# Optimization experiments

Measured on AMD Instinct MI355X. Metric: run time of the kernel, lower is better.

## Reference

```python
import jax, jax.numpy as jnp
import numpy as np

B, QL, KL, D, H = 2, 512, 8192, 1024, 8
HD = D // H  # head dim = 128


def setup_inputs() -> dict:
    key = jax.random.key(0)
    ks = jax.random.split(key, 12)
    s = 0.02
    return {
        "inputs_q": jax.random.normal(ks[0], (B, QL, D), jnp.float32),
        "inputs_k": jax.random.normal(ks[1], (B, KL, D), jnp.float32),
        "inputs_v": jax.random.normal(ks[2], (B, KL, D), jnp.float32),
        "attention_mask": jax.random.randint(ks[3], (B, QL, KL), 0, 2).astype(bool),
        "Wq": jax.random.normal(ks[4], (D, D), jnp.float32) * s,
        "bq": jnp.zeros((D,), jnp.float32),
        "Wk": jax.random.normal(ks[5], (D, D), jnp.float32) * s,
        "bk": jnp.zeros((D,), jnp.float32),
        "Wv": jax.random.normal(ks[6], (D, D), jnp.float32) * s,
        "bv": jnp.zeros((D,), jnp.float32),
        "Wf": jax.random.normal(ks[7], (D, D), jnp.float32) * s,
        "bf": jnp.zeros((D,), jnp.float32),
    }


def reference(inputs_q, inputs_k, inputs_v, attention_mask, Wq, bq, Wk, bk, Wv, bv, Wf, bf):
    # Projections (torch Linear: x @ W.T + b)
    q = inputs_q @ Wq.T + bq  # [B, QL, D]
    k = inputs_k @ Wk.T + bk  # [B, KL, D]
    v = inputs_v @ Wv.T + bv  # [B, KL, D]

    q = q.reshape(B, QL, H, HD)
    k = k.reshape(B, KL, H, HD)
    v = v.reshape(B, KL, H, HD)

    # scores [B, H, QL, KL]
    scores = jnp.einsum("bqhd,bkhd->bhqk", q, k)
    scale = 1.0 / np.sqrt(HD).astype(np.float32)
    scores = scores * scale
    large_k = jnp.float32(1e30)
    scores = jnp.where(attention_mask[:, None, :, :], scores, -large_k)

    probs = jax.nn.softmax(scores, axis=-1)
    # note: original calls self.dropout(normalized) but discards the result -> no-op

    summed = jnp.einsum("bhqk,bkhd->bqhd", probs, v).reshape(B, QL, H * HD)

    # wipe rows whose mask is all zero
    wipe = jnp.all(~attention_mask, axis=2, keepdims=True)  # [B, QL, 1]
    summed = jnp.where(wipe, jnp.zeros_like(summed), summed)

    return summed @ Wf.T + bf
```

## Files before the change

kernel.cpp:

```cpp
#include <hip/hip_runtime.h>
#include <hip/hip_bf16.h>
#include <math.h>

typedef __attribute__((ext_vector_type(4))) float fx4;
typedef __attribute__((ext_vector_type(4))) short sx4;
typedef __attribute__((ext_vector_type(8))) short sx8;
typedef unsigned long long u64;

#define MFMA16(a, b, c) __builtin_amdgcn_mfma_f32_16x16x16bf16_1k(a, b, c, 0, 0, 0)
#define MFMA32(a, b, c) __builtin_amdgcn_mfma_f32_16x16x32_bf16(a, b, c, 0, 0, 0)

__device__ __forceinline__ unsigned short f2bf(float f) {
  unsigned int u = __float_as_uint(f);
  return (unsigned short)((u + 0x7fffu + ((u >> 16) & 1u)) >> 16);
}

typedef const __attribute__((address_space(1))) char* gc1p;
typedef __attribute__((address_space(3))) char* lc3p;
__device__ __forceinline__ void glds16(const void* g, const void* lds_uniform) {
  gc1p gp = (gc1p)(unsigned long long)(uintptr_t)g;
  lc3p lp = (lc3p)(unsigned)__builtin_amdgcn_readfirstlane((int)(unsigned)(uintptr_t)lds_uniform);
  __builtin_amdgcn_global_load_lds(gp, lp, 16, 0, 0);
}

__global__ __launch_bounds__(256) void k_conv(const float* __restrict__ s,
                                              short* __restrict__ d) {
  size_t i = ((size_t)blockIdx.x * 256 + threadIdx.x) * 8;
  const fx4 a = *(const fx4*)(s + i);
  const fx4 b = *(const fx4*)(s + i + 4);
  sx8 o;
  o[0] = (short)f2bf(a[0]); o[1] = (short)f2bf(a[1]);
  o[2] = (short)f2bf(a[2]); o[3] = (short)f2bf(a[3]);
  o[4] = (short)f2bf(b[0]); o[5] = (short)f2bf(b[1]);
  o[6] = (short)f2bf(b[2]); o[7] = (short)f2bf(b[3]);
  *(sx8*)(d + i) = o;
}

__global__ __launch_bounds__(256) void k_conv_a(const float* ink, const float* inq,
                                                const float* Wq, const float* Wk,
                                                const float* Wv, const float* Wf,
                                                short* ck, short* cq, short* cwq,
                                                short* cwk, short* cwv, short* cwf) {
  int bx = blockIdx.x;
  const float* s;
  short* d;
  size_t i;
  if (bx < 8192) {
    s = ink; d = ck; i = (size_t)bx * 2048;
  } else {
    const int r = bx - 8192;
    const int seg = r >> 9;
    s = seg == 0 ? inq : seg == 1 ? Wq : seg == 2 ? Wk : seg == 3 ? Wv : Wf;
    d = seg == 0 ? cq : seg == 1 ? cwq : seg == 2 ? cwk : seg == 3 ? cwv : cwf;
    i = (size_t)(r & 511) * 2048;
  }
  i += (size_t)threadIdx.x * 8;
  const fx4 a = *(const fx4*)(s + i);
  const fx4 b = *(const fx4*)(s + i + 4);
  sx8 o;
  o[0] = (short)f2bf(a[0]); o[1] = (short)f2bf(a[1]);
  o[2] = (short)f2bf(a[2]); o[3] = (short)f2bf(a[3]);
  o[4] = (short)f2bf(b[0]); o[5] = (short)f2bf(b[1]);
  o[6] = (short)f2bf(b[2]); o[7] = (short)f2bf(b[3]);
  *(sx8*)(d + i) = o;
}

__global__ __launch_bounds__(256) void k_pack_mask(const int* __restrict__ mask,
                                                   u64* __restrict__ mb) {
  int g = blockIdx.x * 256 + threadIdx.x;
  u64 bal = __ballot(mask[g] != 0);
  if ((threadIdx.x & 63) == 0) mb[g >> 6] = bal;
}

template <int MODE>
__global__ __launch_bounds__(256) void k_gemm(const short* __restrict__ A,
                                              const short* __restrict__ Bw,
                                              const float* __restrict__ bias,
                                              void* __restrict__ Cptr,
                                              int M, int N, int K, float alpha) {
  __shared__ __align__(16) short sA[8192];
  __shared__ __align__(16) short sB[8192];
  const int t = threadIdx.x;
  const int lane = t & 63;
  const int w = t >> 6;
  const int quad = lane >> 4;
  const int l16 = lane & 15;
  const int x7 = l16 & 7;
  const int ntile = N >> 7;
  const int n0 = (blockIdx.x % ntile) << 7;
  const int m0 = (blockIdx.x / ntile) << 7;
  const int wm = (w >> 1) << 6;
  const int wn = (w & 1) << 6;
  const fx4 fzero = {0.f, 0.f, 0.f, 0.f};
  fx4 acc[4][4];
#pragma unroll
  for (int i = 0; i < 4; i++)
#pragma unroll
    for (int j = 0; j < 4; j++) acc[i][j] = fzero;

  const int srow = (lane >> 3);
  const int scb = lane & 7;

  for (int k0 = 0; k0 < K; k0 += 64) {
    __syncthreads();
#pragma unroll
    for (int j = 0; j < 4; j++) {
      const int row = w * 32 + j * 8 + srow;
      const int cb = scb ^ (row & 7);
      glds16(A + (size_t)(m0 + row) * K + k0 + cb * 8, &sA[(w * 32 + j * 8) * 64]);
      glds16(Bw + (size_t)(n0 + row) * K + k0 + cb * 8, &sB[(w * 32 + j * 8) * 64]);
    }
    __syncthreads();
#pragma unroll
    for (int kc = 0; kc < 2; kc++) {
      const int cbp = ((kc * 4 + quad) ^ x7) * 8;
      sx8 fa[4], fb[4];
#pragma unroll
      for (int i = 0; i < 4; i++) {
        fa[i] = *(const sx8*)(&sA[(wm + i * 16 + l16) * 64 + cbp]);
        fb[i] = *(const sx8*)(&sB[(wn + i * 16 + l16) * 64 + cbp]);
      }
#pragma unroll
      for (int mi = 0; mi < 4; mi++)
#pragma unroll
        for (int ni = 0; ni < 4; ni++)
          acc[mi][ni] = MFMA32(fa[mi], fb[ni], acc[mi][ni]);
    }
  }
#pragma unroll
  for (int ni = 0; ni < 4; ni++) {
    const int col = n0 + wn + ni * 16 + l16;
    const float bval = bias[col];
    if (MODE == 2) {
#pragma unroll
      for (int mi = 0; mi < 4; mi++) {
        const int rowb = m0 + wm + mi * 16 + quad * 4;
        const int bb = rowb >> 13;
        const int kl = (rowb & 8191) ^ ((col & 8) ? 4 : 0);
        sx4 pkv;
#pragma unroll
        for (int r = 0; r < 4; r++) pkv[r] = (short)f2bf(acc[mi][ni][r] + bval);
        *(sx4*)((unsigned short*)Cptr + ((size_t)bb * 1024 + col) * 8192 + kl) = pkv;
      }
    } else {
#pragma unroll
      for (int mi = 0; mi < 4; mi++)
#pragma unroll
        for (int r = 0; r < 4; r++) {
          const int row = m0 + wm + mi * 16 + quad * 4 + r;
          const float v = (acc[mi][ni][r] + bval) * alpha;
          if (MODE == 1) ((float*)Cptr)[(size_t)row * N + col] = v;
          else ((unsigned short*)Cptr)[(size_t)row * N + col] = f2bf(v);
        }
    }
  }
}

__global__ __launch_bounds__(256, 4) void k_attn(const short* __restrict__ Qp,
                                                 const short* __restrict__ Kp,
                                                 const short* __restrict__ Vt,
                                                 const u64* __restrict__ mb,
                                                 float* __restrict__ ml,
                                                 float* __restrict__ Op) {
  __shared__ __align__(16) short sK[8192];
  __shared__ __align__(16) short sV[8192];
  const int x = blockIdx.x;
  const int s = x & 7;
  const int qt = (x >> 3) & 7;
  const int h = (x >> 6) & 7;
  const int b = x >> 9;
  const int t = threadIdx.x;
  const int lane = t & 63;
  const int w = t >> 6;
  const int quad = lane >> 4;
  const int l16 = lane & 15;
  const int x7 = l16 & 7;
  const int q0 = qt << 6;
  const fx4 fzero = {0.f, 0.f, 0.f, 0.f};

  const short* qbase = Qp + (size_t)(b * 512 + q0 + w * 16 + l16) * 1024 + h * 128;
  sx8 aq[4];
#pragma unroll
  for (int kc = 0; kc < 4; kc++) aq[kc] = *(const sx8*)(qbase + kc * 32 + quad * 8);

  fx4 Ot[8];
#pragma unroll
  for (int d = 0; d < 8; d++) Ot[d] = fzero;
  float lsum = 0.f;

  const short* kbase = Kp + (size_t)(b * 8192 + s * 1024) * 1024 + h * 128;
  const short* vbase = Vt + (size_t)(b * 1024 + h * 128) * 8192 + s * 1024;
  const u64* wdp = mb + (size_t)(b * 512 + q0 + w * 16 + l16) * 128 + s * 16;
  const int srow4 = lane >> 4, scb16 = lane & 15;
  const int srow8 = lane >> 3, scb8 = lane & 7;
  const int h4 = ((quad & 1) ^ ((l16 >> 3) & 1)) * 4;

  for (int kt = 0; kt < 16; kt++) {
    __syncthreads();
#pragma unroll
    for (int j = 0; j < 4; j++) {
      const int row = (w * 4 + j) * 4 + srow4;
      const int cb = scb16 ^ (row & 7);
      glds16(kbase + (size_t)(kt * 64 + row) * 1024 + cb * 8, &sK[(w * 4 + j) * 512]);
    }
#pragma unroll
    for (int j = 0; j < 4; j++) {
      const int row = (w * 4 + j) * 8 + srow8;
      const int cb = scb8 ^ (row & 7);
      glds16(vbase + (size_t)row * 8192 + kt * 64 + cb * 8, &sV[(w * 4 + j) * 512]);
    }
    const u64 wd = wdp[kt];
    __syncthreads();
    const unsigned lo = (unsigned)wd, hi = (unsigned)(wd >> 32);
    sx4 pk[4];
#pragma unroll
    for (int nt = 0; nt < 4; nt++) {
      fx4 a = fzero;
#pragma unroll
      for (int kc = 0; kc < 4; kc++) {
        const sx8 kf = *(const sx8*)(&sK[(nt * 16 + l16) * 128 + ((kc * 4 + quad) ^ x7) * 8]);
        a = MFMA32(kf, aq[kc], a);
      }
      const unsigned bits = (nt & 2) ? hi : lo;
      const int sh = (nt & 1) * 16 + quad * 4;
      float pv[4];
#pragma unroll
      for (int r = 0; r < 4; r++) {
        const float e = __builtin_amdgcn_exp2f(a[r]);
        pv[r] = ((bits >> (sh + r)) & 1u) ? e : 0.f;
        lsum += pv[r];
      }
      sx4 pko;
      ((unsigned*)&pko)[0] = __builtin_amdgcn_perm(
          __float_as_uint(pv[1]) + 0x8000u, __float_as_uint(pv[0]) + 0x8000u, 0x07060302u);
      ((unsigned*)&pko)[1] = __builtin_amdgcn_perm(
          __float_as_uint(pv[3]) + 0x8000u, __float_as_uint(pv[2]) + 0x8000u, 0x07060302u);
      pk[nt] = pko;
    }
#pragma unroll
    for (int dt = 0; dt < 8; dt++) {
      fx4 o = Ot[dt];
#pragma unroll
      for (int nt = 0; nt < 4; nt++) {
        const int cb = (2 * nt + (quad >> 1)) ^ x7;
        const sx4 vf = *(const sx4*)(&sV[(dt * 16 + l16) * 64 + cb * 8 + h4]);
        o = MFMA16(vf, pk[nt], o);
      }
      Ot[dt] = o;
    }
  }
  lsum += __shfl_xor(lsum, 16, 64);
  lsum += __shfl_xor(lsum, 32, 64);
  if (lane < 16) ml[(size_t)x * 64 + w * 16 + l16] = lsum;
  float* ob = Op + (size_t)x * 8192 + (w * 16 + l16) * 128 + quad * 4;
#pragma unroll
  for (int dt = 0; dt < 8; dt++) *(fx4*)(ob + dt * 16) = Ot[dt];
}

__global__ __launch_bounds__(256) void k_combine(const float* __restrict__ ml,
                                                 const float* __restrict__ Op,
                                                 short* __restrict__ summed) {
  const int xc = blockIdx.x;
  const int qt = xc & 7;
  const int h = (xc >> 3) & 7;
  const int b = xc >> 6;
  const int t = threadIdx.x;
  const int row = t >> 2;
  const int dg = (t & 3) * 32;
  float L = 0.f;
#pragma unroll
  for (int s = 0; s < 8; s++) L += ml[(size_t)(xc * 8 + s) * 64 + row];
  float o[32];
#pragma unroll
  for (int i = 0; i < 32; i++) o[i] = 0.f;
  if (L != 0.f) {
#pragma unroll
    for (int s = 0; s < 8; s++) {
      const float* src = Op + (size_t)(xc * 8 + s) * 8192 + row * 128 + dg;
#pragma unroll
      for (int i = 0; i < 8; i++) {
        const fx4 v = *(const fx4*)(src + i * 4);
        o[i * 4 + 0] += v[0]; o[i * 4 + 1] += v[1];
        o[i * 4 + 2] += v[2]; o[i * 4 + 3] += v[3];
      }
    }
    const float inv = 1.f / L;
#pragma unroll
    for (int i = 0; i < 32; i++) o[i] *= inv;
  }
  short* dst = summed + (size_t)(b * 512 + qt * 64 + row) * 1024 + h * 128 + dg;
#pragma unroll
  for (int i = 0; i < 4; i++) {
    sx8 pkv;
#pragma unroll
    for (int j = 0; j < 8; j++) pkv[j] = (short)f2bf(o[i * 8 + j]);
    *(sx8*)(dst + i * 8) = pkv;
  }
}

extern "C" void kernel_launch(void* const* d_in, const int* in_sizes, int n_in,
                              void* d_out, int out_size, void* d_ws, size_t ws_size,
                              hipStream_t stream) {
  (void)in_sizes; (void)n_in; (void)out_size; (void)ws_size;
  const float* inq = (const float*)d_in[0];
  const float* ink = (const float*)d_in[1];
  const float* inv = (const float*)d_in[2];
  const int* mask = (const int*)d_in[3];
  const float* Wq = (const float*)d_in[4];
  const float* bq = (const float*)d_in[5];
  const float* Wk = (const float*)d_in[6];
  const float* bk = (const float*)d_in[7];
  const float* Wv = (const float*)d_in[8];
  const float* bv = (const float*)d_in[9];
  const float* Wf = (const float*)d_in[10];
  const float* bf = (const float*)d_in[11];

  char* ws = (char*)d_ws;
  short* S1 = (short*)(ws + 0);
  short* S2 = (short*)(ws + 33554432);
  short* S3 = (short*)(ws + 67108864);
  short* cq = (short*)(ws + 100663296);
  short* cwq = (short*)(ws + 102760448);
  short* cwk = (short*)(ws + 104857600);
  short* cwv = (short*)(ws + 106954752);
  short* cwf = (short*)(ws + 109051904);
  short* Qp = (short*)(ws + 111149056);
  short* summed = (short*)(ws + 113246208);
  u64* mb = (u64*)(ws + 115343360);
  float* ml = (float*)(ws + 116391936);

  const float alpha_q = 0.12751757f;

  k_conv_a<<<10752, 256, 0, stream>>>(ink, inq, Wq, Wk, Wv, Wf, S1, cq, cwq, cwk, cwv, cwf);
  k_pack_mask<<<32768, 256, 0, stream>>>(mask, mb);
  k_gemm<0><<<1024, 256, 0, stream>>>(S1, cwk, bk, S2, 16384, 1024, 1024, 1.f);
  k_conv<<<8192, 256, 0, stream>>>(inv, S1);
  k_gemm<2><<<1024, 256, 0, stream>>>(S1, cwv, bv, S3, 16384, 1024, 1024, 1.f);
  k_gemm<0><<<64, 256, 0, stream>>>(cq, cwq, bq, Qp, 1024, 1024, 1024, alpha_q);
  k_attn<<<1024, 256, 0, stream>>>(Qp, S2, S3, mb, ml, (float*)S1);
  k_combine<<<128, 256, 0, stream>>>(ml, (const float*)S1, summed);
  k_gemm<1><<<64, 256, 0, stream>>>(summed, cwf, bf, (float*)d_out, 1024, 1024, 1024, 1.f);
}
```

Before: 428.1 us.

## Merge prep kernels, fuse V and Q projections, use smaller tiles and remap attention blocks

```diff
diff --git a/kernel.cpp b/kernel.cpp
--- a/kernel.cpp
+++ b/kernel.cpp
@@ -21,6 +21,54 @@
   gc1p gp = (gc1p)(unsigned long long)(uintptr_t)g;
   lc3p lp = (lc3p)(unsigned)__builtin_amdgcn_readfirstlane((int)(unsigned)(uintptr_t)lds_uniform);
   __builtin_amdgcn_global_load_lds(gp, lp, 16, 0, 0);
+}
+
+__global__ __launch_bounds__(256) void k_prep(
+    const float* __restrict__ ink, const float* __restrict__ inq,
+    const float* __restrict__ Wq, const float* __restrict__ Wk,
+    const float* __restrict__ Wv, const float* __restrict__ Wf,
+    const int* __restrict__ mask, short* ck, short* cq, short* cwq, short* cwk,
+    short* cwv, short* cwf, u64* __restrict__ mb) {
+  __shared__ unsigned char nib[256];
+  const int bx = blockIdx.x;
+  const int t = threadIdx.x;
+  if (bx >= 10752) {
+    const int mbx = bx - 10752;
+    const int4 m = *(const int4*)(mask + (size_t)mbx * 1024 + t * 4);
+    nib[t] = (unsigned char)((m.x != 0) | ((m.y != 0) << 1) | ((m.z != 0) << 2) |
+                             ((m.w != 0) << 3));
+    __syncthreads();
+    if (t < 16) {
+      u64 wv = 0;
+#pragma unroll
+      for (int i = 0; i < 16; i++) wv |= (u64)(nib[t * 16 + i] & 0xF) << (4 * i);
+      mb[(size_t)mbx * 16 + t] = wv;
+    }
+    return;
+  }
+  const float* s;
+  short* d;
+  size_t i;
+  if (bx < 8192) {
+    s = ink; d = ck; i = (size_t)bx * 2048;
+  } else if (bx < 8704) {
+    s = inq; d = cq; i = (size_t)(bx - 8192) * 2048;
+  } else {
+    const int r = bx - 8704;
+    const int seg = r >> 9;
+    s = seg == 0 ? Wq : seg == 1 ? Wk : seg == 2 ? Wv : Wf;
+    d = seg == 0 ? cwq : seg == 1 ? cwk : seg == 2 ? cwv : cwf;
+    i = (size_t)(r & 511) * 2048;
+  }
+  i += (size_t)t * 8;
+  const fx4 a = *(const fx4*)(s + i);
+  const fx4 b = *(const fx4*)(s + i + 4);
+  sx8 o;
+  o[0] = (short)f2bf(a[0]); o[1] = (short)f2bf(a[1]);
+  o[2] = (short)f2bf(a[2]); o[3] = (short)f2bf(a[3]);
+  o[4] = (short)f2bf(b[0]); o[5] = (short)f2bf(b[1]);
+  o[6] = (short)f2bf(b[2]); o[7] = (short)f2bf(b[3]);
+  *(sx8*)(d + i) = o;
 }
 
 __global__ __launch_bounds__(256) void k_conv(const float* __restrict__ s,
@@ -36,50 +84,13 @@
   *(sx8*)(d + i) = o;
 }
 
-__global__ __launch_bounds__(256) void k_conv_a(const float* ink, const float* inq,
-                                                const float* Wq, const float* Wk,
-                                                const float* Wv, const float* Wf,
-                                                short* ck, short* cq, short* cwq,
-                                                short* cwk, short* cwv, short* cwf) {
-  int bx = blockIdx.x;
-  const float* s;
-  short* d;
-  size_t i;
-  if (bx < 8192) {
-    s = ink; d = ck; i = (size_t)bx * 2048;
-  } else {
-    const int r = bx - 8192;
-    const int seg = r >> 9;
-    s = seg == 0 ? inq : seg == 1 ? Wq : seg == 2 ? Wk : seg == 3 ? Wv : Wf;
-    d = seg == 0 ? cq : seg == 1 ? cwq : seg == 2 ? cwk : seg == 3 ? cwv : cwf;
-    i = (size_t)(r & 511) * 2048;
-  }
-  i += (size_t)threadIdx.x * 8;
-  const fx4 a = *(const fx4*)(s + i);
-  const fx4 b = *(const fx4*)(s + i + 4);
-  sx8 o;
-  o[0] = (short)f2bf(a[0]); o[1] = (short)f2bf(a[1]);
-  o[2] = (short)f2bf(a[2]); o[3] = (short)f2bf(a[3]);
-  o[4] = (short)f2bf(b[0]); o[5] = (short)f2bf(b[1]);
-  o[6] = (short)f2bf(b[2]); o[7] = (short)f2bf(b[3]);
-  *(sx8*)(d + i) = o;
-}
-
-__global__ __launch_bounds__(256) void k_pack_mask(const int* __restrict__ mask,
-                                                   u64* __restrict__ mb) {
-  int g = blockIdx.x * 256 + threadIdx.x;
-  u64 bal = __ballot(mask[g] != 0);
-  if ((threadIdx.x & 63) == 0) mb[g >> 6] = bal;
-}
-
-template <int MODE>
-__global__ __launch_bounds__(256) void k_gemm(const short* __restrict__ A,
-                                              const short* __restrict__ Bw,
-                                              const float* __restrict__ bias,
-                                              void* __restrict__ Cptr,
-                                              int M, int N, int K, float alpha) {
-  __shared__ __align__(16) short sA[8192];
-  __shared__ __align__(16) short sB[8192];
+template <int MODE, int MT>
+__device__ __forceinline__ void gemm_body(short* sA, short* sB,
+                                          const short* __restrict__ A,
+                                          const short* __restrict__ Bw,
+                                          const float* __restrict__ bias,
+                                          void* __restrict__ Cptr, int M, int N,
+                                          int K, float alpha, int bx) {
   const int t = threadIdx.x;
   const int lane = t & 63;
   const int w = t >> 6;
@@ -87,48 +98,64 @@
   const int l16 = lane & 15;
   const int x7 = l16 & 7;
   const int ntile = N >> 7;
-  const int n0 = (blockIdx.x % ntile) << 7;
-  const int m0 = (blockIdx.x / ntile) << 7;
-  const int wm = (w >> 1) << 6;
-  const int wn = (w & 1) << 6;
+  const int n0 = (bx % ntile) << 7;
+  const int m0 = (bx / ntile) * MT;
+  constexpr int NI = (MT == 128) ? 4 : 2;
+  const int wm = (MT == 128) ? ((w >> 1) << 6) : 0;
+  const int wn = (MT == 128) ? ((w & 1) << 6) : (w << 5);
   const fx4 fzero = {0.f, 0.f, 0.f, 0.f};
-  fx4 acc[4][4];
+  fx4 acc[4][NI];
 #pragma unroll
   for (int i = 0; i < 4; i++)
 #pragma unroll
-    for (int j = 0; j < 4; j++) acc[i][j] = fzero;
-
-  const int srow = (lane >> 3);
+    for (int j = 0; j < NI; j++) acc[i][j] = fzero;
+
+  const int srow = lane >> 3;
   const int scb = lane & 7;
 
   for (int k0 = 0; k0 < K; k0 += 64) {
     __syncthreads();
+    if (MT == 128) {
+#pragma unroll
+      for (int j = 0; j < 4; j++) {
+        const int row = w * 32 + j * 8 + srow;
+        const int cb = scb ^ (row & 7);
+        glds16(A + (size_t)(m0 + row) * K + k0 + cb * 8, &sA[(w * 32 + j * 8) * 64]);
+      }
+    } else {
+#pragma unroll
+      for (int j = 0; j < 2; j++) {
+        const int row = j * 32 + w * 8 + srow;
+        const int cb = scb ^ (row & 7);
+        glds16(A + (size_t)(m0 + row) * K + k0 + cb * 8, &sA[(j * 32 + w * 8) * 64]);
+      }
+    }
 #pragma unroll
     for (int j = 0; j < 4; j++) {
       const int row = w * 32 + j * 8 + srow;
       const int cb = scb ^ (row & 7);
-      glds16(A + (size_t)(m0 + row) * K + k0 + cb * 8, &sA[(w * 32 + j * 8) * 64]);
       glds16(Bw + (size_t)(n0 + row) * K + k0 + cb * 8, &sB[(w * 32 + j * 8) * 64]);
     }
     __syncthreads();
 #pragma unroll
     for (int kc = 0; kc < 2; kc++) {
       const int cbp = ((kc * 4 + quad) ^ x7) * 8;
-      sx8 fa[4], fb[4];
-#pragma unroll
-      for (int i = 0; i < 4; i++) {
+      sx8 fa[4], fb[NI];
+#pragma unroll
+      for (int i = 0; i < 4; i++)
         fa[i] = *(const sx8*)(&sA[(wm + i * 16 + l16) * 64 + cbp]);
+#pragma unroll
+      for (int i = 0; i < NI; i++)
         fb[i] = *(const sx8*)(&sB[(wn + i * 16 + l16) * 64 + cbp]);
-      }
 #pragma unroll
       for (int mi = 0; mi < 4; mi++)
 #pragma unroll
-        for (int ni = 0; ni < 4; ni++)
+        for (int ni = 0; ni < NI; ni++)
           acc[mi][ni] = MFMA32(fa[mi], fb[ni], acc[mi][ni]);
     }
   }
 #pragma unroll
-  for (int ni = 0; ni < 4; ni++) {
+  for (int ni = 0; ni < NI; ni++) {
     const int col = n0 + wn + ni * 16 + l16;
     const float bval = bias[col];
     if (MODE == 2) {
@@ -154,6 +181,39 @@
         }
     }
   }
+}
+
+__global__ __launch_bounds__(256) void k_gemm_k(const short* __restrict__ ck,
+                                                const short* __restrict__ cwk,
+                                                const float* __restrict__ bk,
+                                                short* __restrict__ Kp) {
+  __shared__ __align__(16) short smem[16384];
+  gemm_body<0, 128>(smem, smem + 8192, ck, cwk, bk, Kp, 16384, 1024, 1024, 1.f,
+                    blockIdx.x);
+}
+
+__global__ __launch_bounds__(256) void k_proj_vq(
+    const short* __restrict__ cv, const short* __restrict__ cwv,
+    const float* __restrict__ bv, short* __restrict__ Vt,
+    const short* __restrict__ cq, const short* __restrict__ cwq,
+    const float* __restrict__ bq, short* __restrict__ Qp, float alpha_q) {
+  __shared__ __align__(16) short smem[16384];
+  const int bx = blockIdx.x;
+  if (bx < 128)
+    gemm_body<0, 64>(smem, smem + 8192, cq, cwq, bq, Qp, 1024, 1024, 1024,
+                     alpha_q, bx);
+  else
+    gemm_body<2, 128>(smem, smem + 8192, cv, cwv, bv, Vt, 16384, 1024, 1024,
+                      1.f, bx - 128);
+}
+
+__global__ __launch_bounds__(256) void k_gemm_out(const short* __restrict__ summed,
+                                                  const short* __restrict__ cwf,
+                                                  const float* __restrict__ bf,
+                                                  float* __restrict__ out) {
+  __shared__ __align__(16) short smem[16384];
+  gemm_body<1, 64>(smem, smem + 8192, summed, cwf, bf, out, 1024, 1024, 1024,
+                   1.f, blockIdx.x);
 }
 
 __global__ __launch_bounds__(256, 4) void k_attn(const short* __restrict__ Qp,
@@ -165,10 +225,14 @@
   __shared__ __align__(16) short sK[8192];
   __shared__ __align__(16) short sV[8192];
   const int x = blockIdx.x;
-  const int s = x & 7;
+  const int gl = x & 7;
   const int qt = (x >> 3) & 7;
-  const int h = (x >> 6) & 7;
-  const int b = x >> 9;
+  const int gh = x >> 6;
+  const int g = gh * 8 + gl;
+  const int s = g & 7;
+  const int h = (g >> 3) & 7;
+  const int b = g >> 6;
+  const int li = ((b * 8 + h) * 8 + qt) * 8 + s;
   const int t = threadIdx.x;
   const int lane = t & 63;
   const int w = t >> 6;
@@ -251,8 +315,8 @@
   }
   lsum += __shfl_xor(lsum, 16, 64);
   lsum += __shfl_xor(lsum, 32, 64);
-  if (lane < 16) ml[(size_t)x * 64 + w * 16 + l16] = lsum;
-  float* ob = Op + (size_t)x * 8192 + (w * 16 + l16) * 128 + quad * 4;
+  if (lane < 16) ml[(size_t)li * 64 + w * 16 + l16] = lsum;
+  float* ob = Op + (size_t)li * 8192 + (w * 16 + l16) * 128 + quad * 4;
 #pragma unroll
   for (int dt = 0; dt < 8; dt++) *(fx4*)(ob + dt * 16) = Ot[dt];
 }
@@ -317,8 +381,8 @@
 
   char* ws = (char*)d_ws;
   short* S1 = (short*)(ws + 0);
-  short* S2 = (short*)(ws + 33554432);
-  short* S3 = (short*)(ws + 67108864);
+  short* Kp = (short*)(ws + 33554432);
+  short* Vt = (short*)(ws + 67108864);
   short* cq = (short*)(ws + 100663296);
   short* cwq = (short*)(ws + 102760448);
   short* cwk = (short*)(ws + 104857600);
@@ -331,13 +395,12 @@
 
   const float alpha_q = 0.12751757f;
 
-  k_conv_a<<<10752, 256, 0, stream>>>(ink, inq, Wq, Wk, Wv, Wf, S1, cq, cwq, cwk, cwv, cwf);
-  k_pack_mask<<<32768, 256, 0, stream>>>(mask, mb);
-  k_gemm<0><<<1024, 256, 0, stream>>>(S1, cwk, bk, S2, 16384, 1024, 1024, 1.f);
+  k_prep<<<18944, 256, 0, stream>>>(ink, inq, Wq, Wk, Wv, Wf, mask, S1, cq, cwq,
+                                    cwk, cwv, cwf, mb);
+  k_gemm_k<<<1024, 256, 0, stream>>>(S1, cwk, bk, Kp);
   k_conv<<<8192, 256, 0, stream>>>(inv, S1);
-  k_gemm<2><<<1024, 256, 0, stream>>>(S1, cwv, bv, S3, 16384, 1024, 1024, 1.f);
-  k_gemm<0><<<64, 256, 0, stream>>>(cq, cwq, bq, Qp, 1024, 1024, 1024, alpha_q);
-  k_attn<<<1024, 256, 0, stream>>>(Qp, S2, S3, mb, ml, (float*)S1);
+  k_proj_vq<<<1152, 256, 0, stream>>>(S1, cwv, bv, Vt, cq, cwq, bq, Qp, alpha_q);
+  k_attn<<<1024, 256, 0, stream>>>(Qp, Kp, Vt, mb, ml, (float*)S1);
   k_combine<<<128, 256, 0, stream>>>(ml, (const float*)S1, summed);
-  k_gemm<1><<<64, 256, 0, stream>>>(summed, cwf, bf, (float*)d_out, 1024, 1024, 1024, 1.f);
-}
+  k_gemm_out<<<128, 256, 0, stream>>>(summed, cwf, bf, (float*)d_out);
+}
```

Result: faster. 404.5 us (-5.5%).
